# Kernel tuning notes

Hardware: AMD Instinct MI355X
Metric: run time of the kernel (lower is better)

Reference implementation:

```python
import jax, jax.numpy as jnp
import numpy as np

MINC, MAXC, RATIO = 1, 16, 0.25


def _upsample2x(x):
    # bilinear, align_corners=False, (h,w) -> (2h,2w)
    B, C, h, w = x.shape
    def idx(n_in, n_out):
        src = (jnp.arange(n_out) + 0.5) * (n_in / n_out) - 0.5
        i0f = jnp.floor(src)
        t = (src - i0f).astype(jnp.float32)
        i0 = jnp.clip(i0f, 0, n_in - 1).astype(jnp.int32)
        i1 = jnp.clip(i0f + 1, 0, n_in - 1).astype(jnp.int32)
        return i0, i1, t
    i0, i1, t = idx(h, 2 * h)
    x = x[:, :, i0, :] * (1 - t)[None, None, :, None] + x[:, :, i1, :] * t[None, None, :, None]
    j0, j1, s = idx(w, 2 * w)
    x = x[:, :, :, j0] * (1 - s)[None, None, None, :] + x[:, :, :, j1] * s[None, None, None, :]
    return x


def _connection_counts(x):
    # DFDetector: down(0.5 bilinear, no antialias) == 2x2 avg-pool for even H,W
    B, C, H, W = x.shape
    xd = x.reshape(B, C, H // 2, 2, W // 2, 2).mean(axis=(3, 5))
    xu = _upsample2x(xd)
    df = jnp.abs(x - xu).sum(axis=1)  # [B,H,W]
    dmin = df.reshape(B, -1).min(axis=1)[:, None, None]
    dmax = df.reshape(B, -1).max(axis=1)[:, None, None]
    dn = (df - dmin) / (dmax - dmin + 1e-8)
    return (MINC + jnp.round(dn * (MAXC - MINC))).astype(jnp.int32)  # [B,H,W]


def setup_inputs() -> dict:
    key = jax.random.key(0)
    k0, k1, k2 = jax.random.split(key, 3)
    C = 64
    return {
        "x": jax.random.normal(k0, (2, C, 64, 64), jnp.float32),
        "ln_gamma": jnp.ones((C,), jnp.float32),
        "ln_beta": jnp.zeros((C,), jnp.float32),
        "w1": jax.random.normal(k1, (2 * C, C), jnp.float32) * 0.05,
        "b1": jnp.zeros((2 * C,), jnp.float32),
        "w2": jax.random.normal(k2, (C, 2 * C), jnp.float32) * 0.05,
        "b2": jnp.zeros((C,), jnp.float32),
    }


def reference(x, ln_gamma, ln_beta, w1, b1, w2, b2):
    B, C, H, W = x.shape
    k = _connection_counts(x).reshape(B, H * W)  # [B,HW] in [1,16]

    win = max(3, int(min(H, W) * RATIO))
    win += (win % 2 == 0)  # 17 for 64x64
    half = win // 2
    offs = np.arange(-half, half + 1)
    dy = np.repeat(offs, win); dx = np.tile(offs, win)             # [K2]
    py = np.repeat(np.arange(H), W); px = np.tile(np.arange(W), H)  # [HW]
    ny = py[:, None] + dy[None, :]; nx = px[:, None] + dx[None, :]
    valid = jnp.asarray((ny >= 0) & (ny < H) & (nx >= 0) & (nx < W))          # [HW,K2]
    idx = jnp.asarray(np.clip(ny, 0, H - 1) * W + np.clip(nx, 0, W - 1))      # [HW,K2]

    x_flat = x.transpose(0, 2, 3, 1).reshape(B, H * W, C)
    xn = x_flat / jnp.maximum(jnp.linalg.norm(x_flat, axis=-1, keepdims=True), 1e-12)

    nbr = xn[:, idx]                                   # [B,HW,K2,C]
    sim = jnp.einsum('bpc,bpkc->bpk', xn, nbr)         # cosine similarity
    sim = jnp.where(valid[None], sim, -1e30)           # mask out-of-bounds

    top_sim, top_i = jax.lax.top_k(sim, MAXC)          # [B,HW,16]
    mask = (jnp.arange(MAXC)[None, None, :] < k[:, :, None]).astype(x.dtype)
    wts = jnp.exp(top_sim) * mask
    wts = wts / wts.sum(-1, keepdims=True)

    gidx = jnp.take_along_axis(jnp.broadcast_to(idx[None], (B,) + idx.shape), top_i, axis=2)
    feats = jax.vmap(lambda xf, gi: xf[gi])(x_flat, gidx)  # [B,HW,16,C]
    agg = jnp.einsum('bpk,bpkc->bpc', wts, feats)
    out = agg.reshape(B, H, W, C).transpose(0, 3, 1, 2)

    # per-pixel channel LayerNorm (intent of nn.LayerNorm([C,1,1]))
    mu = x.mean(axis=1, keepdims=True)
    var = ((x - mu) ** 2).mean(axis=1, keepdims=True)
    xln = (x - mu) / jnp.sqrt(var + 1e-5) * ln_gamma[None, :, None, None] + ln_beta[None, :, None, None]

    enh = out + xln
    h1 = jax.nn.relu(jnp.einsum('bchw,dc->bdhw', enh, w1) + b1[None, :, None, None])
    ffn = jnp.einsum('bdhw,cd->bchw', h1, w2) + b2[None, :, None, None]
    return enh + ffn
```

## Files before the change

kernel.cpp:

```cpp
#include <hip/hip_runtime.h>
#include <math.h>

#define BB  2
#define CC  64
#define HH  64
#define WW  64
#define PP  4096
#define CHW 262144
#define KMAX 16
#define NSL 432
#define SSTR 436

#define OFF_XT   0
#define OFF_XNH  524288
#define OFF_XNL  786432
#define OFF_DF   1048576
#define OFF_PMN  1056768
#define OFF_PMX  1057024

typedef __bf16 bf16x8 __attribute__((ext_vector_type(8)));
typedef __bf16 bf16x4 __attribute__((ext_vector_type(4)));
typedef float  f32x4  __attribute__((ext_vector_type(4)));

#define DPP_STEP(v, ctrl, OP) { int _s = __builtin_amdgcn_update_dpp( \
    __float_as_int(v), __float_as_int(v), ctrl, 0xf, 0xf, false); \
    v = OP(v, __int_as_float(_s)); }
__device__ __forceinline__ float addf_(float a, float b) { return a + b; }
__device__ __forceinline__ float wave_max_b(float v) {
    DPP_STEP(v, 0x111, fmaxf) DPP_STEP(v, 0x112, fmaxf) DPP_STEP(v, 0x114, fmaxf)
    DPP_STEP(v, 0x118, fmaxf) DPP_STEP(v, 0x142, fmaxf) DPP_STEP(v, 0x143, fmaxf)
    return __int_as_float(__builtin_amdgcn_readlane(__float_as_int(v), 63));
}
__device__ __forceinline__ float wave_min_b(float v) {
    DPP_STEP(v, 0x111, fminf) DPP_STEP(v, 0x112, fminf) DPP_STEP(v, 0x114, fminf)
    DPP_STEP(v, 0x118, fminf) DPP_STEP(v, 0x142, fminf) DPP_STEP(v, 0x143, fminf)
    return __int_as_float(__builtin_amdgcn_readlane(__float_as_int(v), 63));
}
__device__ __forceinline__ float wave_sum_b(float v) {
    DPP_STEP(v, 0x111, addf_) DPP_STEP(v, 0x112, addf_) DPP_STEP(v, 0x114, addf_)
    DPP_STEP(v, 0x118, addf_) DPP_STEP(v, 0x142, addf_) DPP_STEP(v, 0x143, addf_)
    return __int_as_float(__builtin_amdgcn_readlane(__float_as_int(v), 63));
}

__global__ __launch_bounds__(256) void k_prep(const float* __restrict__ x,
        float* __restrict__ xt,
        unsigned short* __restrict__ xnh, unsigned short* __restrict__ xnl,
        float* __restrict__ df, float* __restrict__ pmn, float* __restrict__ pmx) {
    __shared__ float T[64*33];
    __shared__ float xds[2304];
    __shared__ float pdf[8*33], pss[8*33];
    __shared__ float sinv[32];
    int t = threadIdx.x;
    int bp0 = blockIdx.x * 32;
    int b = bp0 >> 12, p0 = bp0 & 4095;
    int y = p0 >> 6, x0 = p0 & 63;
    const float* xb = x + b*CHW + p0;
    #pragma unroll
    for (int i = 0; i < 8; ++i) {
        int idx = t + i*256;
        int c = idx >> 5, pxl = idx & 31;
        T[c*33 + pxl] = xb[c*PP + pxl];
    }
    int m = y >> 1;
    int R0, R1; float ty;
    if ((y & 1) == 0) { R0 = m > 0 ? m-1 : 0; R1 = m; ty = 0.75f; }
    else              { R0 = m; R1 = m < 31 ? m+1 : 31; ty = 0.25f; }
    int h0 = x0 >> 1;
    #pragma unroll
    for (int i = 0; i < 9; ++i) {
        int id = t + i*256;
        int c = id / 36, rem = id - c*36;
        int rr = (rem >= 18) ? 1 : 0, cc = rem - rr*18;
        int row = rr ? R1 : R0;
        int col = h0 - 1 + cc; col = col < 0 ? 0 : (col > 31 ? 31 : col);
        const float* xp = x + b*CHW + c*PP + row*2*WW + col*2;
        xds[id] = (xp[0] + xp[1] + xp[WW] + xp[WW+1]) * 0.25f;
    }
    __syncthreads();
    int px = t & 31, sl = t >> 5;
    int xxp = x0 + px;
    int n2 = xxp >> 1, jx0, jx1; float tx;
    if ((xxp & 1) == 0) { jx0 = n2 > 0 ? n2-1 : 0; jx1 = n2; tx = 0.75f; }
    else                { jx0 = n2; jx1 = n2 < 31 ? n2+1 : 31; tx = 0.25f; }
    int cc0 = jx0 - h0 + 1, cc1 = jx1 - h0 + 1;
    float dfa = 0.f, ss = 0.f;
    #pragma unroll
    for (int ci = 0; ci < 8; ++ci) {
        int c = sl*8 + ci;
        const float* xc = &xds[c*36];
        float a00 = xc[cc0],      a10 = xc[18 + cc0];
        float a01 = xc[cc1],      a11 = xc[18 + cc1];
        float r0 = a00*(1.f-ty) + a10*ty;
        float r1 = a01*(1.f-ty) + a11*ty;
        float xu = r0*(1.f-tx) + r1*tx;
        float v = T[c*33 + px];
        dfa += fabsf(v - xu);
        ss  += v*v;
    }
    pdf[sl*33 + px] = dfa; pss[sl*33 + px] = ss;
    __syncthreads();
    if (t < 32) {
        float d = 0.f, s = 0.f;
        #pragma unroll
        for (int q = 0; q < 8; ++q) { d += pdf[q*33 + t]; s += pss[q*33 + t]; }
        df[bp0 + t] = d;
        sinv[t] = 1.f / fmaxf(sqrtf(s), 1e-12f);
        float mn = d, mx = d;
        #pragma unroll
        for (int off = 1; off < 32; off <<= 1) {
            mn = fminf(mn, __shfl_xor(mn, off));
            mx = fmaxf(mx, __shfl_xor(mx, off));
        }
        if (t == 0) { pmn[blockIdx.x] = mn; pmx[blockIdx.x] = mx; }
    }
    __syncthreads();
    int px2 = t >> 3, cg = t & 7;
    float inv = sinv[px2];
    int bp = bp0 + px2;
    float4 f0, f1; bf16x8 hh, ll;
    #pragma unroll
    for (int k = 0; k < 8; ++k) {
        float v = T[(cg*8 + k)*33 + px2];
        if (k < 4) ((float*)&f0)[k] = v; else ((float*)&f1)[k-4] = v;
        float xnv = v * inv;
        __bf16 hb = (__bf16)xnv;
        float lo = xnv - (float)hb;
        hh[k] = hb; ll[k] = (__bf16)lo;
    }
    *(float4*)&xt[bp*64 + cg*8]     = f0;
    *(float4*)&xt[bp*64 + cg*8 + 4] = f1;
    *(bf16x8*)&xnh[bp*64 + cg*8] = hh;
    *(bf16x8*)&xnl[bp*64 + cg*8] = ll;
}

__global__ __launch_bounds__(1024) void k_fuse(
        const unsigned short* __restrict__ xnh,
        const unsigned short* __restrict__ xnl,
        const float* __restrict__ xt, const float* __restrict__ df,
        const float* __restrict__ pmn, const float* __restrict__ pmx,
        const float* __restrict__ gamma, const float* __restrict__ beta,
        const float* __restrict__ w1, const float* __restrict__ b1,
        const float* __restrict__ w2, const float* __restrict__ b2,
        float* __restrict__ out) {
    __shared__ float  simsL[16*SSTR];
    __shared__ __bf16 w1bf[128*72];
    __shared__ __bf16 w2bf[64*136];
    __shared__ __bf16 enh16[16*72];
    __shared__ __bf16 h1bf[16*136];
    __shared__ float  enhT32[16*68];
    __shared__ float  smm[2];
    int t = threadIdx.x;
    int bid = blockIdx.x;
    int b = bid >> 8, tyi = (bid >> 3) & 31, txi = bid & 7;
    int y0 = tyi*2, x0 = txi*8;
    int pbase = (b << 12) + y0*64 + x0;
    int pix0 = pbase & 4095;
    int wv = t >> 6, lane = t & 63;
    int lr = lane & 15, lq = lane >> 4;
    #pragma unroll
    for (int j = 0; j < 2; ++j) {
        int i4 = t + j*1024;
        float4 v = *(const float4*)(w1 + i4*4);
        int dd = i4 >> 4, c0 = (i4 & 15)*4;
        bf16x4 h; h[0]=(__bf16)v.x; h[1]=(__bf16)v.y; h[2]=(__bf16)v.z; h[3]=(__bf16)v.w;
        *(bf16x4*)&w1bf[dd*72 + c0] = h;
    }
    #pragma unroll
    for (int j = 0; j < 2; ++j) {
        int i4 = t + j*1024;
        float4 v = *(const float4*)(w2 + i4*4);
        int cc2 = i4 >> 5, d0 = (i4 & 31)*4;
        bf16x4 h; h[0]=(__bf16)v.x; h[1]=(__bf16)v.y; h[2]=(__bf16)v.z; h[3]=(__bf16)v.w;
        *(bf16x4*)&w2bf[cc2*136 + d0] = h;
    }
    if (t < 64) {
        float v = fminf(pmn[b*128 + t], pmn[b*128 + 64 + t]);
        v = wave_min_b(v);
        if (t == 0) smm[0] = v;
    } else if (t < 128) {
        int u = t & 63;
        float v = fmaxf(pmx[b*128 + u], pmx[b*128 + 64 + u]);
        v = wave_max_b(v);
        if (u == 0) smm[1] = v;
    }
    {
        int bpA = pbase + ((lr >> 3) << 6) + (lr & 7);
        const unsigned short* ah = xnh + bpA*64 + lq*8;
        const unsigned short* al = xnl + bpA*64 + lq*8;
        bf16x8 ah0 = *(const bf16x8*)ah, ah1 = *(const bf16x8*)(ah + 32);
        bf16x8 al0 = *(const bf16x8*)al, al1 = *(const bf16x8*)(al + 32);
        for (int nt = wv; nt < 27; nt += 16) {
            int S = nt*16 + lr;
            int rr = S / 24, cc = S - rr*24;
            int ny = y0 + rr - 8, nx = x0 + cc - 8;
            bool vimg = ((unsigned)ny < 64u) && ((unsigned)nx < 64u);
            int bq = vimg ? ((b << 12) + ny*64 + nx) : pbase;
            const unsigned short* bh = xnh + bq*64 + lq*8;
            const unsigned short* bl = xnl + bq*64 + lq*8;
            bf16x8 bh0 = *(const bf16x8*)bh, bh1 = *(const bf16x8*)(bh + 32);
            bf16x8 bl0 = *(const bf16x8*)bl, bl1 = *(const bf16x8*)(bl + 32);
            f32x4 acc = (f32x4){0.f,0.f,0.f,0.f};
            acc = __builtin_amdgcn_mfma_f32_16x16x32_bf16(ah0, bh0, acc, 0, 0, 0);
            acc = __builtin_amdgcn_mfma_f32_16x16x32_bf16(ah0, bl0, acc, 0, 0, 0);
            acc = __builtin_amdgcn_mfma_f32_16x16x32_bf16(al0, bh0, acc, 0, 0, 0);
            acc = __builtin_amdgcn_mfma_f32_16x16x32_bf16(ah1, bh1, acc, 0, 0, 0);
            acc = __builtin_amdgcn_mfma_f32_16x16x32_bf16(ah1, bl1, acc, 0, 0, 0);
            acc = __builtin_amdgcn_mfma_f32_16x16x32_bf16(al1, bh1, acc, 0, 0, 0);
            #pragma unroll
            for (int r = 0; r < 4; ++r) {
                int pxo = lq*4 + r;
                simsL[pxo*SSTR + S] = vimg ? acc[r] : -1e30f;
            }
        }
    }
    __syncthreads();
    {
        int i_loc = wv >> 3, j_loc = wv & 7;
        int bp = pbase + i_loc*64 + j_loc;
        const float* srow = &simsL[wv*SSTR];
        float tv[7];
        #pragma unroll
        for (int j = 0; j < 7; ++j) {
            int s = lane + (j << 6);
            bool in = (j < 6) || (lane < 48);
            int rr = s / 24, cc = s - rr*24;
            int sy = rr - i_loc, sx = cc - j_loc;
            bool ok = in && ((unsigned)sy <= 16u) && ((unsigned)sx <= 16u);
            tv[j] = ok ? srow[s] : -1e30f;
        }
        float lbv = tv[0]; int lbj = 0;
        #pragma unroll
        for (int j = 1; j < 7; ++j) if (tv[j] > lbv) { lbv = tv[j]; lbj = j; }
        float dmin = smm[0], dmax = smm[1];
        float dn = (df[bp] - dmin) / (dmax - dmin + 1e-8f);
        int kk = 1 + (int)rintf(dn * 15.f);
        float S = 0.f, acc = 0.f;
        for (int rnd = 0; rnd < kk; ++rnd) {
            float bv = wave_max_b(lbv);
            unsigned long long msk = __ballot(lbv == bv);
            int src = __ffsll(msk) - 1;
            int js = __builtin_amdgcn_readlane(lbj, src);
            int s = src + (js << 6);
            int rr = s / 24, cc = s - rr*24;
            int q = pbase + (rr - 8)*64 + (cc - 8);
            float e = expf(bv);
            S += e;
            acc += e * xt[q*64 + lane];
            if (lane == src) {
                #pragma unroll
                for (int j = 0; j < 7; ++j) if (j == lbj) tv[j] = -3e30f;
            }
            lbv = tv[0]; lbj = 0;
            #pragma unroll
            for (int j = 1; j < 7; ++j) if (tv[j] > lbv) { lbv = tv[j]; lbj = j; }
        }
        float xv = xt[bp*64 + lane];
        float mu = wave_sum_b(xv) * (1.f/64.f);
        float d = xv - mu;
        float var = wave_sum_b(d*d) * (1.f/64.f);
        float xln = d / sqrtf(var + 1e-5f) * gamma[lane] + beta[lane];
        float val = acc / S + xln;
        enhT32[wv*68 + lane] = val;
        enh16[wv*72 + lane] = (__bf16)val;
    }
    __syncthreads();
    if (wv < 8) {
        int d0 = wv*16;
        f32x4 acc1 = (f32x4){0.f,0.f,0.f,0.f};
        #pragma unroll
        for (int kh = 0; kh < 2; ++kh) {
            int kb = kh*32 + lq*8;
            bf16x8 a  = *(bf16x8*)&enh16[lr*72 + kb];
            bf16x8 bb = *(bf16x8*)&w1bf[(d0 + lr)*72 + kb];
            acc1 = __builtin_amdgcn_mfma_f32_16x16x32_bf16(a, bb, acc1, 0, 0, 0);
        }
        int dd = d0 + lr;
        float bias = b1[dd];
        #pragma unroll
        for (int r = 0; r < 4; ++r) {
            int pxr = lq*4 + r;
            h1bf[pxr*136 + dd] = (__bf16)fmaxf(acc1[r] + bias, 0.f);
        }
    }
    __syncthreads();
    if (wv < 4) {
        int c0 = wv*16;
        f32x4 acc2 = (f32x4){0.f,0.f,0.f,0.f};
        #pragma unroll
        for (int kh = 0; kh < 4; ++kh) {
            int kb = kh*32 + lq*8;
            bf16x8 a  = *(bf16x8*)&h1bf[lr*136 + kb];
            bf16x8 bb = *(bf16x8*)&w2bf[(c0 + lr)*136 + kb];
            acc2 = __builtin_amdgcn_mfma_f32_16x16x32_bf16(a, bb, acc2, 0, 0, 0);
        }
        int c = c0 + lr;
        float bias = b2[c];
        #pragma unroll
        for (int r = 0; r < 4; ++r) {
            int pxr = lq*4 + r;
            int pix = pix0 + ((pxr >> 3) << 6) + (pxr & 7);
            out[b*CHW + c*PP + pix] = acc2[r] + bias + enhT32[pxr*68 + c];
        }
    }
}

extern "C" void kernel_launch(void* const* d_in, const int* in_sizes, int n_in,
                              void* d_out, int out_size, void* d_ws, size_t ws_size,
                              hipStream_t stream) {
    const float* x     = (const float*)d_in[0];
    const float* gamma = (const float*)d_in[1];
    const float* beta  = (const float*)d_in[2];
    const float* w1    = (const float*)d_in[3];
    const float* b1    = (const float*)d_in[4];
    const float* w2    = (const float*)d_in[5];
    const float* b2    = (const float*)d_in[6];
    float* ws  = (float*)d_ws;
    float* xt  = ws + OFF_XT;
    float* df  = ws + OFF_DF;
    float* pmn = ws + OFF_PMN;
    float* pmx = ws + OFF_PMX;
    unsigned short* xnh = (unsigned short*)(ws + OFF_XNH);
    unsigned short* xnl = (unsigned short*)(ws + OFF_XNL);
    float* out = (float*)d_out;

    k_prep<<<256, 256, 0, stream>>>(x, xt, xnh, xnl, df, pmn, pmx);
    k_fuse<<<512, 1024, 0, stream>>>(xnh, xnl, xt, df, pmn, pmx, gamma, beta,
                                     w1, b1, w2, b2, out);
}
```

Baseline: 34.72 us.

## Use 4x4 pixel tiles and precompute bf16 weights in prep kernel

Changes each fused block's tile from 2x8 to 4x4 pixels. The neighbour window shrinks from 24x18 to 20x20 (400 slots), so fewer similarity MFMA tiles are computed per block. The bf16 conversion of w1/w2 moves out of every k_fuse block into two extra k_prep blocks that write to workspace, and the FFN reads the weights from global memory instead of LDS. It also switches expf to __expf and fixes the top-k removal index (js vs lbj), which slightly changes numerics.

Result: slower. 36.77 us (+5.9%).

```diff
diff --git a/kernel.cpp b/kernel.cpp
--- a/kernel.cpp
+++ b/kernel.cpp
@@ -8,8 +8,8 @@
 #define PP  4096
 #define CHW 262144
 #define KMAX 16
-#define NSL 432
-#define SSTR 436
+#define NSL 400
+#define SSTR 452
 
 #define OFF_XT   0
 #define OFF_XNH  524288
@@ -17,6 +17,8 @@
 #define OFF_DF   1048576
 #define OFF_PMN  1056768
 #define OFF_PMX  1057024
+#define OFF_W1B  1057280
+#define OFF_W2B  1061376
 
 typedef __bf16 bf16x8 __attribute__((ext_vector_type(8)));
 typedef __bf16 bf16x4 __attribute__((ext_vector_type(4)));
@@ -45,7 +47,22 @@
 __global__ __launch_bounds__(256) void k_prep(const float* __restrict__ x,
         float* __restrict__ xt,
         unsigned short* __restrict__ xnh, unsigned short* __restrict__ xnl,
-        float* __restrict__ df, float* __restrict__ pmn, float* __restrict__ pmx) {
+        float* __restrict__ df, float* __restrict__ pmn, float* __restrict__ pmx,
+        const float* __restrict__ w1, const float* __restrict__ w2,
+        unsigned short* __restrict__ w1b, unsigned short* __restrict__ w2b) {
+    if (blockIdx.x >= 256) {
+        const float* wsrc = (blockIdx.x == 256) ? w1 : w2;
+        unsigned short* wdst = (blockIdx.x == 256) ? w1b : w2b;
+        int t = threadIdx.x;
+        #pragma unroll
+        for (int j = 0; j < 8; ++j) {
+            int i4 = t + j*256;
+            float4 v = *(const float4*)(wsrc + i4*4);
+            bf16x4 h; h[0]=(__bf16)v.x; h[1]=(__bf16)v.y; h[2]=(__bf16)v.z; h[3]=(__bf16)v.w;
+            *(bf16x4*)&wdst[i4*4] = h;
+        }
+        return;
+    }
     __shared__ float T[64*33];
     __shared__ float xds[2304];
     __shared__ float pdf[8*33], pss[8*33];
@@ -139,40 +156,23 @@
         const float* __restrict__ xt, const float* __restrict__ df,
         const float* __restrict__ pmn, const float* __restrict__ pmx,
         const float* __restrict__ gamma, const float* __restrict__ beta,
-        const float* __restrict__ w1, const float* __restrict__ b1,
-        const float* __restrict__ w2, const float* __restrict__ b2,
+        const unsigned short* __restrict__ w1b, const float* __restrict__ b1,
+        const unsigned short* __restrict__ w2b, const float* __restrict__ b2,
         float* __restrict__ out) {
     __shared__ float  simsL[16*SSTR];
-    __shared__ __bf16 w1bf[128*72];
-    __shared__ __bf16 w2bf[64*136];
     __shared__ __bf16 enh16[16*72];
     __shared__ __bf16 h1bf[16*136];
     __shared__ float  enhT32[16*68];
     __shared__ float  smm[2];
     int t = threadIdx.x;
     int bid = blockIdx.x;
-    int b = bid >> 8, tyi = (bid >> 3) & 31, txi = bid & 7;
-    int y0 = tyi*2, x0 = txi*8;
+    int b = bid >> 8, tid = bid & 255;
+    int tyi = tid >> 4, txi = tid & 15;
+    int y0 = tyi*4, x0 = txi*4;
     int pbase = (b << 12) + y0*64 + x0;
     int pix0 = pbase & 4095;
     int wv = t >> 6, lane = t & 63;
     int lr = lane & 15, lq = lane >> 4;
-    #pragma unroll
-    for (int j = 0; j < 2; ++j) {
-        int i4 = t + j*1024;
-        float4 v = *(const float4*)(w1 + i4*4);
-        int dd = i4 >> 4, c0 = (i4 & 15)*4;
-        bf16x4 h; h[0]=(__bf16)v.x; h[1]=(__bf16)v.y; h[2]=(__bf16)v.z; h[3]=(__bf16)v.w;
-        *(bf16x4*)&w1bf[dd*72 + c0] = h;
-    }
-    #pragma unroll
-    for (int j = 0; j < 2; ++j) {
-        int i4 = t + j*1024;
-        float4 v = *(const float4*)(w2 + i4*4);
-        int cc2 = i4 >> 5, d0 = (i4 & 31)*4;
-        bf16x4 h; h[0]=(__bf16)v.x; h[1]=(__bf16)v.y; h[2]=(__bf16)v.z; h[3]=(__bf16)v.w;
-        *(bf16x4*)&w2bf[cc2*136 + d0] = h;
-    }
     if (t < 64) {
         float v = fminf(pmn[b*128 + t], pmn[b*128 + 64 + t]);
         v = wave_min_b(v);
@@ -184,14 +184,14 @@
         if (u == 0) smm[1] = v;
     }
     {
-        int bpA = pbase + ((lr >> 3) << 6) + (lr & 7);
+        int bpA = pbase + ((lr >> 2) << 6) + (lr & 3);
         const unsigned short* ah = xnh + bpA*64 + lq*8;
         const unsigned short* al = xnl + bpA*64 + lq*8;
         bf16x8 ah0 = *(const bf16x8*)ah, ah1 = *(const bf16x8*)(ah + 32);
         bf16x8 al0 = *(const bf16x8*)al, al1 = *(const bf16x8*)(al + 32);
-        for (int nt = wv; nt < 27; nt += 16) {
+        for (int nt = wv; nt < 25; nt += 16) {
             int S = nt*16 + lr;
-            int rr = S / 24, cc = S - rr*24;
+            int rr = S / 20, cc = S - rr*20;
             int ny = y0 + rr - 8, nx = x0 + cc - 8;
             bool vimg = ((unsigned)ny < 64u) && ((unsigned)nx < 64u);
             int bq = vimg ? ((b << 12) + ny*64 + nx) : pbase;
@@ -215,15 +215,15 @@
     }
     __syncthreads();
     {
-        int i_loc = wv >> 3, j_loc = wv & 7;
+        int i_loc = wv >> 2, j_loc = wv & 3;
         int bp = pbase + i_loc*64 + j_loc;
         const float* srow = &simsL[wv*SSTR];
         float tv[7];
         #pragma unroll
         for (int j = 0; j < 7; ++j) {
             int s = lane + (j << 6);
-            bool in = (j < 6) || (lane < 48);
-            int rr = s / 24, cc = s - rr*24;
+            bool in = (s < NSL);
+            int rr = s / 20, cc = s - rr*20;
             int sy = rr - i_loc, sx = cc - j_loc;
             bool ok = in && ((unsigned)sy <= 16u) && ((unsigned)sx <= 16u);
             tv[j] = ok ? srow[s] : -1e30f;
@@ -241,14 +241,14 @@
             int src = __ffsll(msk) - 1;
             int js = __builtin_amdgcn_readlane(lbj, src);
             int s = src + (js << 6);
-            int rr = s / 24, cc = s - rr*24;
+            int rr = s / 20, cc = s - rr*20;
             int q = pbase + (rr - 8)*64 + (cc - 8);
-            float e = expf(bv);
+            float e = __expf(bv);
             S += e;
             acc += e * xt[q*64 + lane];
             if (lane == src) {
                 #pragma unroll
-                for (int j = 0; j < 7; ++j) if (j == lbj) tv[j] = -3e30f;
+                for (int j = 0; j < 7; ++j) if (j == js) tv[j] = -3e30f;
             }
             lbv = tv[0]; lbj = 0;
             #pragma unroll
@@ -271,7 +271,7 @@
         for (int kh = 0; kh < 2; ++kh) {
             int kb = kh*32 + lq*8;
             bf16x8 a  = *(bf16x8*)&enh16[lr*72 + kb];
-            bf16x8 bb = *(bf16x8*)&w1bf[(d0 + lr)*72 + kb];
+            bf16x8 bb = *(const bf16x8*)&w1b[(d0 + lr)*64 + kb];
             acc1 = __builtin_amdgcn_mfma_f32_16x16x32_bf16(a, bb, acc1, 0, 0, 0);
         }
         int dd = d0 + lr;
@@ -290,7 +290,7 @@
         for (int kh = 0; kh < 4; ++kh) {
             int kb = kh*32 + lq*8;
             bf16x8 a  = *(bf16x8*)&h1bf[lr*136 + kb];
-            bf16x8 bb = *(bf16x8*)&w2bf[(c0 + lr)*136 + kb];
+            bf16x8 bb = *(const bf16x8*)&w2b[(c0 + lr)*128 + kb];
             acc2 = __builtin_amdgcn_mfma_f32_16x16x32_bf16(a, bb, acc2, 0, 0, 0);
         }
         int c = c0 + lr;
@@ -298,7 +298,7 @@
         #pragma unroll
         for (int r = 0; r < 4; ++r) {
             int pxr = lq*4 + r;
-            int pix = pix0 + ((pxr >> 3) << 6) + (pxr & 7);
+            int pix = pix0 + ((pxr >> 2) << 6) + (pxr & 3);
             out[b*CHW + c*PP + pix] = acc2[r] + bias + enhT32[pxr*68 + c];
         }
     }
@@ -321,9 +321,11 @@
     float* pmx = ws + OFF_PMX;
     unsigned short* xnh = (unsigned short*)(ws + OFF_XNH);
     unsigned short* xnl = (unsigned short*)(ws + OFF_XNL);
+    unsigned short* w1b = (unsigned short*)(ws + OFF_W1B);
+    unsigned short* w2b = (unsigned short*)(ws + OFF_W2B);
     float* out = (float*)d_out;
 
-    k_prep<<<256, 256, 0, stream>>>(x, xt, xnh, xnl, df, pmn, pmx);
+    k_prep<<<258, 256, 0, stream>>>(x, xt, xnh, xnl, df, pmn, pmx, w1, w2, w1b, w2b);
     k_fuse<<<512, 1024, 0, stream>>>(xnh, xnl, xt, df, pmn, pmx, gamma, beta,
-                                     w1, b1, w2, b2, out);
-}
+                                     w1b, b1, w2b, b2, out);
+}
```
